# Optimization experiments

Measured on AMD Instinct MI355X. Metric: run time of the kernel, lower is better.

Reference implementation:

```python
import jax, jax.numpy as jnp
import numpy as np

B, S, D, H, HD = 4, 2048, 1024, 16, 64  # batch, seq, d_model, heads, head_dim


def setup_inputs() -> dict:
    key = jax.random.key(0)
    ks = jax.random.split(key, 9)
    scale = 0.02
    x = jax.random.normal(ks[0], (B, S, D), jnp.float32)
    Wq = jax.random.normal(ks[1], (D, H, HD), jnp.float32) * scale
    Wk = jax.random.normal(ks[2], (D, H, HD), jnp.float32) * scale
    Wv = jax.random.normal(ks[3], (D, H, HD), jnp.float32) * scale
    bq = jax.random.normal(ks[4], (H, HD), jnp.float32) * scale
    bk = jax.random.normal(ks[5], (H, HD), jnp.float32) * scale
    bv = jax.random.normal(ks[6], (H, HD), jnp.float32) * scale
    Wo = jax.random.normal(ks[7], (H, HD, D), jnp.float32) * scale
    bo = jax.random.normal(ks[8], (D,), jnp.float32) * scale
    return {"x": x, "Wq": Wq, "bq": bq, "Wk": Wk, "bk": bk,
            "Wv": Wv, "bv": bv, "Wo": Wo, "bo": bo}


def reference(x, Wq, bq, Wk, bk, Wv, bv, Wo, bo):
    # QKV projections -> (B, S, H, HD)
    q = jnp.einsum("bsd,dhe->bshe", x, Wq) + bq
    k = jnp.einsum("bsd,dhe->bshe", x, Wk) + bk
    v = jnp.einsum("bsd,dhe->bshe", x, Wv) + bv
    # scaled dot-product attention (deterministic, no mask/bias)
    q = q / jnp.sqrt(jnp.asarray(HD, q.dtype))
    scores = jnp.einsum("bqhd,bkhd->bhqk", q, k)  # (B, H, S, S)
    attn = jax.nn.softmax(scores, axis=-1)
    ctx = jnp.einsum("bhqk,bkhd->bqhd", attn, v)  # (B, S, H, HD)
    # output projection -> (B, S, D)
    return jnp.einsum("bqhd,hdo->bqo", ctx, Wo) + bo
```

## Files before the change

kernel.cpp:

```cpp
#include <hip/hip_runtime.h>


typedef unsigned short u16;
typedef __attribute__((ext_vector_type(4))) float f32x4;
typedef __attribute__((ext_vector_type(8))) short s16x8;
typedef __attribute__((ext_vector_type(4))) unsigned short u16x4;
typedef __attribute__((ext_vector_type(2))) unsigned int u32x2;
typedef __attribute__((ext_vector_type(4))) unsigned int u32x4;

#define DEV __device__ __forceinline__

#if __has_builtin(__builtin_amdgcn_exp2f)
#define EXP2(x) __builtin_amdgcn_exp2f(x)
#else
#define EXP2(x) exp2f(x)
#endif

DEV u16 f2b(float f) {
  unsigned u = __float_as_uint(f);
  u += 0x7fffu + ((u >> 16) & 1u);
  return (u16)(u >> 16);
}

DEV unsigned pack2(float a, float b) {
#if __has_builtin(__builtin_amdgcn_cvt_pk_bf16_f32)
  typedef __attribute__((ext_vector_type(2))) __bf16 bf16x2;
  bf16x2 r = __builtin_amdgcn_cvt_pk_bf16_f32(a, b);
  return __builtin_bit_cast(unsigned, r);
#else
  return (unsigned)f2b(a) | ((unsigned)f2b(b) << 16);
#endif
}

DEV void async16(const void* g, void* l) {
  __builtin_amdgcn_global_load_lds(
      (const __attribute__((address_space(1))) unsigned int*)g,
      (__attribute__((address_space(3))) unsigned int*)l, 16, 0, 0);
}

__global__ void k_cast(const float* __restrict__ x, u16* __restrict__ xb) {
  int i = (blockIdx.x * 256 + threadIdx.x) * 4;
  float4 v = *(const float4*)(x + i);
  u16x4 o;
  o.x = f2b(v.x); o.y = f2b(v.y); o.z = f2b(v.z); o.w = f2b(v.w);
  *(u16x4*)(xb + i) = o;
}

__global__ void k_packw_all(const float* __restrict__ Wq, const float* __restrict__ Wk,
                            const float* __restrict__ Wv, const float* __restrict__ Wo,
                            u16* __restrict__ wt, u16* __restrict__ wot, float qscale) {
  const float* src; u16* dst; float scale = 1.0f;
  switch (blockIdx.z) {
    case 0: src = Wq; dst = wt; scale = qscale; break;
    case 1: src = Wk; dst = wt + 1024 * 1024; break;
    case 2: src = Wv; dst = wt + 2 * 1024 * 1024; break;
    default: src = Wo; dst = wot; break;
  }
  __shared__ float tile[32][33];
  int t = threadIdx.x;
  int k0 = blockIdx.x * 32, n0 = blockIdx.y * 32;
  int c = t & 31, r0 = t >> 5;
#pragma unroll
  for (int p = 0; p < 4; ++p) {
    int r = p * 8 + r0;
    tile[r][c] = src[(size_t)(k0 + r) * 1024 + n0 + c] * scale;
  }
  __syncthreads();
#pragma unroll
  for (int p = 0; p < 4; ++p) {
    int r = p * 8 + r0;
    dst[(size_t)(n0 + r) * 1024 + k0 + c] = f2b(tile[c][r]);
  }
}

__global__ void k_packbias(const float* __restrict__ bq, const float* __restrict__ bk,
                           const float* __restrict__ bv, float* __restrict__ out,
                           float qscale) {
  int t = blockIdx.x * 256 + threadIdx.x;
  float v = (t < 1024) ? bq[t] * qscale : (t < 2048 ? bk[t - 1024] : bv[t - 2048]);
  out[t] = v;
}

template <int MODE>
__global__ __launch_bounds__(256, 2) void k_gemm_bt(
    const u16* __restrict__ A, const u16* __restrict__ Bt,
    const float* __restrict__ bias, void* __restrict__ Cout,
    int K, int ldC, int nbase) {
  __shared__ u16 As[128 * 64];
  __shared__ u16 Bs[128 * 64];
  const int t = threadIdx.x;
  const int w = t >> 6, l = t & 63;
  const int lane15 = l & 15, quad = l >> 4;
  const int m0 = blockIdx.x * 128, n0 = nbase + blockIdx.y * 128;
  const int wm = (w >> 1) * 64, wn = (w & 1) * 64;

  const int srow = t >> 3, cp = t & 7;
  const u16* aSrc[4]; const u16* bSrc[4]; int ldsOff[4];
#pragma unroll
  for (int i = 0; i < 4; ++i) {
    int row = i * 32 + srow;
    int gc = cp ^ (row & 7);
    aSrc[i] = A + (size_t)(m0 + row) * K + gc * 8;
    bSrc[i] = Bt + (size_t)(n0 + row) * K + gc * 8;
    ldsOff[i] = (i * 32 + w * 8) * 64;
  }

  f32x4 acc[4][4] = {};

  for (int kk = 0; kk < K; kk += 64) {
#pragma unroll
    for (int i = 0; i < 4; ++i) async16(aSrc[i] + kk, As + ldsOff[i]);
#pragma unroll
    for (int i = 0; i < 4; ++i) async16(bSrc[i] + kk, Bs + ldsOff[i]);
    __builtin_amdgcn_s_waitcnt(0);
    __syncthreads();

#pragma unroll
    for (int ks = 0; ks < 2; ++ks) {
      s16x8 af[4], bf[4];
#pragma unroll
      for (int mi = 0; mi < 4; ++mi) {
        int r = wm + mi * 16 + lane15;
        int c = ks * 4 + quad;
        af[mi] = *(const s16x8*)(As + r * 64 + (c ^ (r & 7)) * 8);
      }
#pragma unroll
      for (int ni = 0; ni < 4; ++ni) {
        int r = wn + ni * 16 + lane15;
        int c = ks * 4 + quad;
        bf[ni] = *(const s16x8*)(Bs + r * 64 + (c ^ (r & 7)) * 8);
      }
#pragma unroll
      for (int mi = 0; mi < 4; ++mi)
#pragma unroll
        for (int ni = 0; ni < 4; ++ni)
          acc[mi][ni] = (MODE == 2)
              ? __builtin_amdgcn_mfma_f32_16x16x32_bf16(af[mi], bf[ni], acc[mi][ni], 0, 0, 0)
              : __builtin_amdgcn_mfma_f32_16x16x32_bf16(bf[ni], af[mi], acc[mi][ni], 0, 0, 0);
    }
    __syncthreads();
  }

  if (MODE == 2) {
#pragma unroll
    for (int ni = 0; ni < 4; ++ni) {
      int gn = n0 + wn + ni * 16 + lane15;
      float bb = bias[gn];
      int gv = gn - 2048;
      int hh = gv >> 6, hd = gv & 63;
#pragma unroll
      for (int mi = 0; mi < 4; ++mi) {
        int gmBase = m0 + wm + mi * 16 + quad * 4;
        int bb2 = gmBase >> 11, s = gmBase & 2047;
        u32x2 o;
        o.x = pack2(acc[mi][ni][0] + bb, acc[mi][ni][1] + bb);
        o.y = pack2(acc[mi][ni][2] + bb, acc[mi][ni][3] + bb);
        *(u32x2*)((u16*)Cout + (((size_t)(bb2 * 16 + hh) * 64 + hd) * 2048 + s)) = o;
      }
    }
  } else {
#pragma unroll
    for (int ni = 0; ni < 4; ++ni) {
      int gnb = n0 + wn + ni * 16 + quad * 4;
      float4 bb = *(const float4*)(bias + gnb);
#pragma unroll
      for (int mi = 0; mi < 4; ++mi) {
        int gm = m0 + wm + mi * 16 + lane15;
        if (MODE == 0) {
          u32x2 o;
          o.x = pack2(acc[mi][ni][0] + bb.x, acc[mi][ni][1] + bb.y);
          o.y = pack2(acc[mi][ni][2] + bb.z, acc[mi][ni][3] + bb.w);
          *(u32x2*)((u16*)Cout + (size_t)gm * ldC + gnb) = o;
        } else {
          float4 v;
          v.x = acc[mi][ni][0] + bb.x; v.y = acc[mi][ni][1] + bb.y;
          v.z = acc[mi][ni][2] + bb.z; v.w = acc[mi][ni][3] + bb.w;
          *(float4*)((float*)Cout + (size_t)gm * ldC + gnb) = v;
        }
      }
    }
  }
}

__global__ __launch_bounds__(256, 4) void k_flash(
    const u16* __restrict__ qkv, const u16* __restrict__ vt, u16* __restrict__ ctx) {
  __shared__ u16 Ks[128 * 64];
  __shared__ u16 Vs[64 * 128];
  const int t = threadIdx.x;
  const int w = t >> 6, l = t & 63;
  const int lane15 = l & 15, quad = l >> 4;
  const int qt = blockIdx.x, bh = blockIdx.y;
  const int b = bh >> 4, h = bh & 15;

  const int qrow = b * 2048 + qt * 64 + w * 16 + lane15;
  const u16* qp = qkv + (size_t)qrow * 2048 + h * 64 + quad * 8;
  s16x8 qf0 = *(const s16x8*)qp;
  s16x8 qf1 = *(const s16x8*)(qp + 32);

  const int srow = t >> 3, cp = t & 7;
  const u16* kSrc[4]; const u16* vSrc[4]; int ldsOff[4];
#pragma unroll
  for (int i = 0; i < 4; ++i) {
    int krow = i * 32 + srow;
    int xk = (krow & 3) | (((krow >> 3) & 1) << 2);
    kSrc[i] = qkv + (size_t)(b * 2048 + krow) * 2048 + 1024 + h * 64 + (cp ^ xk) * 8;
    int vrow = i * 16 + w * 4 + quad;
    vSrc[i] = vt + (size_t)bh * (64 * 2048) + (size_t)vrow * 2048 + (lane15 ^ (vrow & 7)) * 8;
    ldsOff[i] = (i * 32 + w * 8) * 64;
  }

  const int kr = (lane15 >> 2) * 8 + (lane15 & 3);
  f32x4 O[4] = {};
  f32x4 sacc = {};
  const u32x4 onesu = {0x3F803F80u, 0x3F803F80u, 0x3F803F80u, 0x3F803F80u};
  const s16x8 onesf = __builtin_bit_cast(s16x8, onesu);

  for (int jt = 0; jt < 16; ++jt) {
    const size_t kAdv = (size_t)jt * 128 * 2048;
    const int vAdv = jt * 128;
#pragma unroll
    for (int i = 0; i < 4; ++i) async16(kSrc[i] + kAdv, Ks + ldsOff[i]);
#pragma unroll
    for (int i = 0; i < 4; ++i) async16(vSrc[i] + vAdv, Vs + ldsOff[i]);
    __builtin_amdgcn_s_waitcnt(0);
    __syncthreads();

    f32x4 st[8] = {};
#pragma unroll
    for (int ks2 = 0; ks2 < 2; ++ks2) {
      s16x8 qf = ks2 ? qf1 : qf0;
#pragma unroll
      for (int tt = 0; tt < 8; ++tt) {
        int rr = kr + (tt & 1) * 4 + (tt >> 1) * 32;
        int xk = (rr & 3) | (((rr >> 3) & 1) << 2);
        s16x8 kf = *(const s16x8*)(Ks + rr * 64 + ((ks2 * 4 + quad) ^ xk) * 8);
        st[tt] = __builtin_amdgcn_mfma_f32_16x16x32_bf16(kf, qf, st[tt], 0, 0, 0);
      }
    }

#pragma unroll
    for (int ks = 0; ks < 4; ++ks) {
      float p0 = EXP2(st[2 * ks][0]), p1 = EXP2(st[2 * ks][1]);
      float p2 = EXP2(st[2 * ks][2]), p3 = EXP2(st[2 * ks][3]);
      float p4 = EXP2(st[2 * ks + 1][0]), p5 = EXP2(st[2 * ks + 1][1]);
      float p6 = EXP2(st[2 * ks + 1][2]), p7 = EXP2(st[2 * ks + 1][3]);
      u32x4 pu = {pack2(p0, p1), pack2(p2, p3), pack2(p4, p5), pack2(p6, p7)};
      s16x8 pf = __builtin_bit_cast(s16x8, pu);
      sacc = __builtin_amdgcn_mfma_f32_16x16x32_bf16(onesf, pf, sacc, 0, 0, 0);
#pragma unroll
      for (int co = 0; co < 4; ++co) {
        int rr = co * 16 + lane15;
        s16x8 vf = *(const s16x8*)(Vs + rr * 128 + (((ks * 4 + quad) ^ (rr & 7))) * 8);
        O[co] = __builtin_amdgcn_mfma_f32_16x16x32_bf16(vf, pf, O[co], 0, 0, 0);
      }
    }
    __syncthreads();
  }

  float inv = 1.0f / sacc[0];
#pragma unroll
  for (int co = 0; co < 4; ++co) {
    u32x2 o;
    o.x = pack2(O[co][0] * inv, O[co][1] * inv);
    o.y = pack2(O[co][2] * inv, O[co][3] * inv);
    *(u32x2*)(ctx + (size_t)qrow * 1024 + h * 64 + co * 16 + quad * 4) = o;
  }
}

static constexpr size_t OFF_XB  = 0;
static constexpr size_t OFF_WT  = OFF_XB + (16u << 20);
static constexpr size_t OFF_WOT = OFF_WT + (6u << 20);
static constexpr size_t OFF_B3  = OFF_WOT + (2u << 20);
static constexpr size_t OFF_QKV = OFF_B3 + (1u << 20);
static constexpr size_t OFF_VT  = OFF_QKV + (32u << 20);
static constexpr size_t OFF_CTX = OFF_VT + (16u << 20);

extern "C" void kernel_launch(void* const* d_in, const int* in_sizes, int n_in,
                              void* d_out, int out_size, void* d_ws, size_t ws_size,
                              hipStream_t stream) {
  const float* x  = (const float*)d_in[0];
  const float* Wq = (const float*)d_in[1];
  const float* bq = (const float*)d_in[2];
  const float* Wk = (const float*)d_in[3];
  const float* bk = (const float*)d_in[4];
  const float* Wv = (const float*)d_in[5];
  const float* bv = (const float*)d_in[6];
  const float* Wo = (const float*)d_in[7];
  const float* bo = (const float*)d_in[8];
  char* ws = (char*)d_ws;
  u16* xb    = (u16*)(ws + OFF_XB);
  u16* wt    = (u16*)(ws + OFF_WT);
  u16* wot   = (u16*)(ws + OFF_WOT);
  float* b3  = (float*)(ws + OFF_B3);
  u16* qkv   = (u16*)(ws + OFF_QKV);
  u16* vtb   = (u16*)(ws + OFF_VT);
  u16* ctx   = (u16*)(ws + OFF_CTX);
  float* out = (float*)d_out;

  const float QSCALE = 0.125f * 1.44269504f;

  k_cast<<<8192, 256, 0, stream>>>(x, xb);
  k_packw_all<<<dim3(32, 32, 4), 256, 0, stream>>>(Wq, Wk, Wv, Wo, wt, wot, QSCALE);
  k_packbias<<<12, 256, 0, stream>>>(bq, bk, bv, b3, QSCALE);
  k_gemm_bt<0><<<dim3(64, 16), 256, 0, stream>>>(xb, wt, b3, qkv, 1024, 2048, 0);
  k_gemm_bt<2><<<dim3(64, 8), 256, 0, stream>>>(xb, wt, b3, vtb, 1024, 2048, 2048);
  k_flash<<<dim3(32, 64), 256, 0, stream>>>(qkv, vtb, ctx);
  k_gemm_bt<1><<<dim3(64, 8), 256, 0, stream>>>(ctx, wot, bo, out, 1024, 1024, 0);
}
```

Baseline: 292.2 us.

## Double-buffer flash K/V tiles and merge QK and V projection GEMMs

The flash-attention kernel now uses two shared-memory buffers for K/V, prefetching the next tile while computing the current one. This removes the trailing barrier and lowers launch bounds to 2 blocks per SM because LDS use doubles. The QK and V projection GEMMs are fused into one launch, with a per-block branch choosing the transposed V store. The non-V epilogue also switches from vectorized stores to scalar per-element stores, which may reduce store efficiency.

Measured after the change: 295.8 us. No clear change (+1.2%).

```diff
diff --git a/kernel.cpp b/kernel.cpp
--- a/kernel.cpp
+++ b/kernel.cpp
@@ -81,17 +81,17 @@
   out[t] = v;
 }
 
-template <int MODE>
+template <bool OUT_BF16>
 __global__ __launch_bounds__(256, 2) void k_gemm_bt(
     const u16* __restrict__ A, const u16* __restrict__ Bt,
-    const float* __restrict__ bias, void* __restrict__ Cout,
-    int K, int ldC, int nbase) {
+    const float* __restrict__ bias, void* __restrict__ Cout, u16* __restrict__ VT,
+    int K, int ldC, int nsplit) {
   __shared__ u16 As[128 * 64];
   __shared__ u16 Bs[128 * 64];
   const int t = threadIdx.x;
   const int w = t >> 6, l = t & 63;
   const int lane15 = l & 15, quad = l >> 4;
-  const int m0 = blockIdx.x * 128, n0 = nbase + blockIdx.y * 128;
+  const int m0 = blockIdx.x * 128, n0 = blockIdx.y * 128;
   const int wm = (w >> 1) * 64, wn = (w & 1) * 64;
 
   const int srow = t >> 3, cp = t & 7;
@@ -134,19 +134,31 @@
       for (int mi = 0; mi < 4; ++mi)
 #pragma unroll
         for (int ni = 0; ni < 4; ++ni)
-          acc[mi][ni] = (MODE == 2)
-              ? __builtin_amdgcn_mfma_f32_16x16x32_bf16(af[mi], bf[ni], acc[mi][ni], 0, 0, 0)
-              : __builtin_amdgcn_mfma_f32_16x16x32_bf16(bf[ni], af[mi], acc[mi][ni], 0, 0, 0);
+          acc[mi][ni] = __builtin_amdgcn_mfma_f32_16x16x32_bf16(af[mi], bf[ni], acc[mi][ni], 0, 0, 0);
     }
     __syncthreads();
   }
 
-  if (MODE == 2) {
-#pragma unroll
-    for (int ni = 0; ni < 4; ++ni) {
-      int gn = n0 + wn + ni * 16 + lane15;
-      float bb = bias[gn];
-      int gv = gn - 2048;
+  const bool vpath = (VT != nullptr) && (n0 >= nsplit);
+#pragma unroll
+  for (int ni = 0; ni < 4; ++ni) {
+    int gn = n0 + wn + ni * 16 + lane15;
+    float bb = bias[gn];
+    if (!vpath) {
+#pragma unroll
+      for (int mi = 0; mi < 4; ++mi) {
+        int gmBase = m0 + wm + mi * 16 + quad * 4;
+#pragma unroll
+        for (int r = 0; r < 4; ++r) {
+          float v = acc[mi][ni][r] + bb;
+          if (OUT_BF16)
+            ((u16*)Cout)[(size_t)(gmBase + r) * ldC + gn] = f2b(v);
+          else
+            ((float*)Cout)[(size_t)(gmBase + r) * ldC + gn] = v;
+        }
+      }
+    } else {
+      int gv = gn - nsplit;
       int hh = gv >> 6, hd = gv & 63;
 #pragma unroll
       for (int mi = 0; mi < 4; ++mi) {
@@ -155,37 +167,15 @@
         u32x2 o;
         o.x = pack2(acc[mi][ni][0] + bb, acc[mi][ni][1] + bb);
         o.y = pack2(acc[mi][ni][2] + bb, acc[mi][ni][3] + bb);
-        *(u32x2*)((u16*)Cout + (((size_t)(bb2 * 16 + hh) * 64 + hd) * 2048 + s)) = o;
-      }
-    }
-  } else {
-#pragma unroll
-    for (int ni = 0; ni < 4; ++ni) {
-      int gnb = n0 + wn + ni * 16 + quad * 4;
-      float4 bb = *(const float4*)(bias + gnb);
-#pragma unroll
-      for (int mi = 0; mi < 4; ++mi) {
-        int gm = m0 + wm + mi * 16 + lane15;
-        if (MODE == 0) {
-          u32x2 o;
-          o.x = pack2(acc[mi][ni][0] + bb.x, acc[mi][ni][1] + bb.y);
-          o.y = pack2(acc[mi][ni][2] + bb.z, acc[mi][ni][3] + bb.w);
-          *(u32x2*)((u16*)Cout + (size_t)gm * ldC + gnb) = o;
-        } else {
-          float4 v;
-          v.x = acc[mi][ni][0] + bb.x; v.y = acc[mi][ni][1] + bb.y;
-          v.z = acc[mi][ni][2] + bb.z; v.w = acc[mi][ni][3] + bb.w;
-          *(float4*)((float*)Cout + (size_t)gm * ldC + gnb) = v;
-        }
-      }
-    }
-  }
-}
-
-__global__ __launch_bounds__(256, 4) void k_flash(
+        *(u32x2*)(VT + (((size_t)(bb2 * 16 + hh) * 64 + hd) * 2048 + s)) = o;
+      }
+    }
+  }
+}
+
+__global__ __launch_bounds__(256, 2) void k_flash(
     const u16* __restrict__ qkv, const u16* __restrict__ vt, u16* __restrict__ ctx) {
-  __shared__ u16 Ks[128 * 64];
-  __shared__ u16 Vs[64 * 128];
+  __shared__ u16 S[2][16384];
   const int t = threadIdx.x;
   const int w = t >> 6, l = t & 63;
   const int lane15 = l & 15, quad = l >> 4;
@@ -198,15 +188,16 @@
   s16x8 qf1 = *(const s16x8*)(qp + 32);
 
   const int srow = t >> 3, cp = t & 7;
-  const u16* kSrc[4]; const u16* vSrc[4]; int ldsOff[4];
+  const u16* kSrc[4]; const u16* vSrc[4]; int kOff[4]; int vOff[4];
 #pragma unroll
   for (int i = 0; i < 4; ++i) {
     int krow = i * 32 + srow;
     int xk = (krow & 3) | (((krow >> 3) & 1) << 2);
     kSrc[i] = qkv + (size_t)(b * 2048 + krow) * 2048 + 1024 + h * 64 + (cp ^ xk) * 8;
-    int vrow = i * 16 + w * 4 + quad;
-    vSrc[i] = vt + (size_t)bh * (64 * 2048) + (size_t)vrow * 2048 + (lane15 ^ (vrow & 7)) * 8;
-    ldsOff[i] = (i * 32 + w * 8) * 64;
+    kOff[i] = (i * 32 + w * 8) * 64;
+    int vr = (i >> 1) * 32 + srow;
+    vSrc[i] = vt + (size_t)bh * (64 * 2048) + (size_t)vr * 2048 + (i & 1) * 64 + (cp ^ (vr & 7)) * 8;
+    vOff[i] = 8192 + (i & 1) * 4096 + (i >> 1) * 2048 + w * 512;
   }
 
   const int kr = (lane15 >> 2) * 8 + (lane15 & 3);
@@ -215,15 +206,24 @@
   const u32x4 onesu = {0x3F803F80u, 0x3F803F80u, 0x3F803F80u, 0x3F803F80u};
   const s16x8 onesf = __builtin_bit_cast(s16x8, onesu);
 
+#pragma unroll
+  for (int i = 0; i < 4; ++i) async16(kSrc[i], &S[0][kOff[i]]);
+#pragma unroll
+  for (int i = 0; i < 4; ++i) async16(vSrc[i], &S[0][vOff[i]]);
+
   for (int jt = 0; jt < 16; ++jt) {
-    const size_t kAdv = (size_t)jt * 128 * 2048;
-    const int vAdv = jt * 128;
-#pragma unroll
-    for (int i = 0; i < 4; ++i) async16(kSrc[i] + kAdv, Ks + ldsOff[i]);
-#pragma unroll
-    for (int i = 0; i < 4; ++i) async16(vSrc[i] + vAdv, Vs + ldsOff[i]);
     __builtin_amdgcn_s_waitcnt(0);
     __syncthreads();
+    const u16* Sb = S[jt & 1];
+    if (jt < 15) {
+      const size_t kAdv = (size_t)(jt + 1) * 128 * 2048;
+      const int vAdv = (jt + 1) * 128;
+      u16* D = S[(jt & 1) ^ 1];
+#pragma unroll
+      for (int i = 0; i < 4; ++i) async16(kSrc[i] + kAdv, D + kOff[i]);
+#pragma unroll
+      for (int i = 0; i < 4; ++i) async16(vSrc[i] + vAdv, D + vOff[i]);
+    }
 
     f32x4 st[8] = {};
 #pragma unroll
@@ -233,7 +233,7 @@
       for (int tt = 0; tt < 8; ++tt) {
         int rr = kr + (tt & 1) * 4 + (tt >> 1) * 32;
         int xk = (rr & 3) | (((rr >> 3) & 1) << 2);
-        s16x8 kf = *(const s16x8*)(Ks + rr * 64 + ((ks2 * 4 + quad) ^ xk) * 8);
+        s16x8 kf = *(const s16x8*)(Sb + rr * 64 + ((ks2 * 4 + quad) ^ xk) * 8);
         st[tt] = __builtin_amdgcn_mfma_f32_16x16x32_bf16(kf, qf, st[tt], 0, 0, 0);
       }
     }
@@ -247,14 +247,15 @@
       u32x4 pu = {pack2(p0, p1), pack2(p2, p3), pack2(p4, p5), pack2(p6, p7)};
       s16x8 pf = __builtin_bit_cast(s16x8, pu);
       sacc = __builtin_amdgcn_mfma_f32_16x16x32_bf16(onesf, pf, sacc, 0, 0, 0);
+      const u16* Vh = Sb + 8192 + (ks >> 1) * 4096;
+      int c7 = (ks & 1) * 4 + quad;
 #pragma unroll
       for (int co = 0; co < 4; ++co) {
         int rr = co * 16 + lane15;
-        s16x8 vf = *(const s16x8*)(Vs + rr * 128 + (((ks * 4 + quad) ^ (rr & 7))) * 8);
+        s16x8 vf = *(const s16x8*)(Vh + rr * 64 + ((c7 ^ (rr & 7))) * 8);
         O[co] = __builtin_amdgcn_mfma_f32_16x16x32_bf16(vf, pf, O[co], 0, 0, 0);
       }
     }
-    __syncthreads();
   }
 
   float inv = 1.0f / sacc[0];
@@ -302,8 +303,7 @@
   k_cast<<<8192, 256, 0, stream>>>(x, xb);
   k_packw_all<<<dim3(32, 32, 4), 256, 0, stream>>>(Wq, Wk, Wv, Wo, wt, wot, QSCALE);
   k_packbias<<<12, 256, 0, stream>>>(bq, bk, bv, b3, QSCALE);
-  k_gemm_bt<0><<<dim3(64, 16), 256, 0, stream>>>(xb, wt, b3, qkv, 1024, 2048, 0);
-  k_gemm_bt<2><<<dim3(64, 8), 256, 0, stream>>>(xb, wt, b3, vtb, 1024, 2048, 2048);
+  k_gemm_bt<true><<<dim3(64, 24), 256, 0, stream>>>(xb, wt, b3, qkv, vtb, 1024, 2048, 2048);
   k_flash<<<dim3(32, 64), 256, 0, stream>>>(qkv, vtb, ctx);
-  k_gemm_bt<1><<<dim3(64, 8), 256, 0, stream>>>(ctx, wot, bo, out, 1024, 1024, 0);
-}
+  k_gemm_bt<false><<<dim3(64, 8), 256, 0, stream>>>(ctx, wot, bo, out, nullptr, 1024, 1024, 1 << 30);
+}
```
